# Kernel tuning notes

Hardware: AMD Instinct MI355X
Metric: run time of the kernel (lower is better)

Reference implementation:

```python
import jax, jax.numpy as jnp
import numpy as np

SIZES = [6890, 1723, 431, 108, 27]
P = [s + 1 for s in SIZES]  # padding vertex at each level
SPIRAL = 9
ENC_IN = [3, 16, 32, 64]; ENC_OUT = [16, 32, 64, 128]
DEC_IN = [128, 64, 32, 32, 16]; DEC_OUT = [64, 32, 32, 16, 3]
LATENT = 128
B = 64


def setup_inputs() -> dict:
    ks = iter(jax.random.split(jax.random.key(0), 80))
    def nrm(shape, scale=1.0):
        return jax.random.normal(next(ks), shape, dtype=jnp.float32) * scale
    inp = {'x': nrm((B, P[0], 3))}
    for l in range(4):
        inp['S%d' % l] = jax.random.randint(next(ks), (P[l], SPIRAL), 0, P[l], dtype=jnp.int32)
        inp['D%d' % l] = nrm((P[l + 1], P[l]), float(1.0 / np.sqrt(P[l])))
        inp['U%d' % l] = nrm((P[l], P[l + 1]), float(1.0 / np.sqrt(P[l + 1])))
    for i, (ci, co) in enumerate(zip(ENC_IN, ENC_OUT)):
        inp['W_e%d' % i] = nrm((ci * SPIRAL, co), float(1.0 / np.sqrt(ci * SPIRAL)))
        inp['b_e%d' % i] = nrm((co,), 0.02)
    inp['W_fe'] = nrm((P[4] * ENC_OUT[-1], LATENT), float(1.0 / np.sqrt(P[4] * ENC_OUT[-1])))
    inp['b_fe'] = nrm((LATENT,), 0.02)
    inp['W_fd'] = nrm((LATENT, P[4] * DEC_IN[0]), float(1.0 / np.sqrt(LATENT)))
    inp['b_fd'] = nrm((P[4] * DEC_IN[0],), 0.02)
    for i, (ci, co) in enumerate(zip(DEC_IN, DEC_OUT)):
        inp['W_d%d' % i] = nrm((ci * SPIRAL, co), float(1.0 / np.sqrt(ci * SPIRAL)))
        inp['b_d%d' % i] = nrm((co,), 0.02)
    return inp


def _sconv(x, idx, W, b, act):
    # spiral gather: x[B,P,F], idx[P,S] -> [B,P,S*F]; Linear + activation + zero last (padding) vertex
    Bn, Pn, F = x.shape
    g = x[:, idx, :].reshape(Bn, Pn, -1)
    y = act(g @ W + b)
    return y.at[:, -1, :].set(0.0)


def _forward(x, S, D, U, We, be, W_fe, b_fe, W_fd, b_fd, Wd, bd):
    elu = jax.nn.elu
    h = x
    for i in range(4):  # encoder: spiral conv then downsample
        h = _sconv(h, S[i], We[i], be[i], elu)
        h = jnp.einsum('pq,bqf->bpf', D[i], h)
    z = h.reshape(h.shape[0], -1) @ W_fe + b_fe
    h = (z @ W_fd + b_fd).reshape(z.shape[0], P[4], DEC_IN[0])
    for i in range(4):  # decoder: upsample then spiral conv
        h = jnp.einsum('pq,bqf->bpf', U[3 - i], h)
        h = _sconv(h, S[3 - i], Wd[i], bd[i], elu)
    h = _sconv(h, S[0], Wd[4], bd[4], lambda v: v)  # final identity-activation conv to xyz
    return h, z


def reference(x, S0, S1, S2, S3, D0, D1, D2, D3, U0, U1, U2, U3,
              W_e0, b_e0, W_e1, b_e1, W_e2, b_e2, W_e3, b_e3,
              W_fe, b_fe, W_fd, b_fd,
              W_d0, b_d0, W_d1, b_d1, W_d2, b_d2, W_d3, b_d3, W_d4, b_d4):
    return _forward(x, [S0, S1, S2, S3], [D0, D1, D2, D3], [U0, U1, U2, U3],
                    [W_e0, W_e1, W_e2, W_e3], [b_e0, b_e1, b_e2, b_e3],
                    W_fe, b_fe, W_fd, b_fd,
                    [W_d0, W_d1, W_d2, W_d3, W_d4], [b_d0, b_d1, b_d2, b_d3, b_d4])
```

## Files before the change

kernel.cpp:

```cpp
#include <hip/hip_runtime.h>
#include <math.h>

typedef unsigned short u16;
typedef _Float16 f16;
typedef __attribute__((ext_vector_type(8))) _Float16 f16x8;
typedef __attribute__((ext_vector_type(4))) float f32x4;
typedef float4 __attribute__((aligned(4))) float4u;

constexpr int P0 = 6891, P1 = 1724, P2 = 432, P3 = 109, P4 = 28;
constexpr int P0p = 6912;

constexpr size_t OFF_ZB   = 0;
constexpr size_t OFF_MD0  = OFF_ZB   + 256;
constexpr size_t OFF_MU0  = OFF_MD0  + (size_t)1792 * 6912 * 2;
constexpr size_t OFF_MD1  = OFF_MU0  + (size_t)6912 * 1792 * 2;
constexpr size_t OFF_MU1  = OFF_MD1  + (size_t)512 * 1792 * 2;
constexpr size_t OFF_MD2  = OFF_MU1  + (size_t)1792 * 512 * 2;
constexpr size_t OFF_MU2  = OFF_MD2  + (size_t)128 * 512 * 2;
constexpr size_t OFF_MD3  = OFF_MU2  + (size_t)512 * 128 * 2;
constexpr size_t OFF_MU3  = OFF_MD3  + (size_t)128 * 128 * 2;
constexpr size_t OFF_WE1  = OFF_MU3  + (size_t)128 * 128 * 2;
constexpr size_t OFF_WE2  = OFF_WE1  + (size_t)32 * 192 * 2;
constexpr size_t OFF_WE3  = OFF_WE2  + (size_t)64 * 320 * 2;
constexpr size_t OFF_WD0  = OFF_WE3  + (size_t)128 * 576 * 2;
constexpr size_t OFF_WD1  = OFF_WD0  + (size_t)64 * 1152 * 2;
constexpr size_t OFF_WD2  = OFF_WD1  + (size_t)32 * 576 * 2;
constexpr size_t OFF_WD3  = OFF_WD2  + (size_t)32 * 320 * 2;
constexpr size_t OFF_XT   = OFF_WD3  + (size_t)16 * 320 * 2;
constexpr size_t OFF_FCP  = OFF_XT   + (size_t)6912 * 64 * 3 * 4;
constexpr size_t OFF_B0   = OFF_FCP  + (size_t)28 * 8192 * 4;
constexpr size_t OFF_B1   = OFF_B0   + (size_t)1024 * 6912 * 2;
constexpr size_t OFF_PB   = OFF_B1   + (size_t)6912 * 2048 * 2;
constexpr size_t OFF_END  = OFF_PB   + (size_t)14680064;

constexpr int CN_MD0 = 1792 * 864, CN_MU0 = 6912 * 224, CN_MD1 = 512 * 224,
              CN_MU1 = 1792 * 64, CN_MD2 = 128 * 64, CN_MU2 = 512 * 16,
              CN_MD3 = 128 * 16, CN_MU3 = 128 * 16,
              CN_W1 = 32 * 24, CN_W2 = 64 * 40, CN_W3 = 128 * 72,
              CN_V0 = 64 * 144, CN_V1 = 32 * 72, CN_V2 = 32 * 40, CN_V3 = 16 * 40,
              CN_XT = 6912 * 64, CN_ZB = 32;
constexpr int CN_TOTAL = CN_MD0 + CN_MU0 + CN_MD1 + CN_MU1 + CN_MD2 + CN_MU2 +
                         CN_MD3 + CN_MU3 + CN_W1 + CN_W2 + CN_W3 + CN_V0 + CN_V1 +
                         CN_V2 + CN_V3 + CN_XT + CN_ZB;

__device__ __forceinline__ u16 f2h(float v) {
  f16 h = (f16)v;
  return __builtin_bit_cast(u16, h);
}
__device__ __forceinline__ float h2f(u16 u) {
  return (float)__builtin_bit_cast(f16, u);
}
__device__ __forceinline__ float eluf(float v) { return v > 0.f ? v : expm1f(v); }

__device__ __forceinline__ void gload16(const void* g, void* lds) {
  __builtin_amdgcn_global_load_lds(
      (const __attribute__((address_space(1))) unsigned int*)g,
      (__attribute__((address_space(3))) unsigned int*)lds, 16, 0, 0);
}

struct PrepSrc {
  const float *D0, *U0, *D1, *U1, *D2, *U2, *D3, *U3;
  const float *We1, *We2, *We3, *Wd0, *Wd1, *Wd2, *Wd3;
  const float *x;
};

__device__ __forceinline__ void conv_m_item(const float* __restrict__ M, u16* __restrict__ out,
                                            int idx, int P, int Q, int Qpad) {
  int cpr = Qpad >> 3;
  int p = idx / cpr, cq = idx - p * cpr;
  int w0 = (cq << 3) & ~63;
  int q0 = w0 + (((cq & 7) ^ (p & 7)) << 3);
  uint4 pk;
  if (p < P && q0 + 8 <= Q) {
    const float* s = M + (size_t)p * Q + q0;
    float4 va = *(const float4u*)s;
    float4 vb = *(const float4u*)(s + 4);
    pk.x = f2h(va.x) | ((unsigned)f2h(va.y) << 16);
    pk.y = f2h(va.z) | ((unsigned)f2h(va.w) << 16);
    pk.z = f2h(vb.x) | ((unsigned)f2h(vb.y) << 16);
    pk.w = f2h(vb.z) | ((unsigned)f2h(vb.w) << 16);
  } else {
    u16 v[8];
#pragma unroll
    for (int j = 0; j < 8; ++j) {
      int q = q0 + j;
      float f = (p < P && q < Q) ? M[(size_t)p * Q + q] : 0.f;
      v[j] = f2h(f);
    }
    pk.x = v[0] | ((unsigned)v[1] << 16); pk.y = v[2] | ((unsigned)v[3] << 16);
    pk.z = v[4] | ((unsigned)v[5] << 16); pk.w = v[6] | ((unsigned)v[7] << 16);
  }
  *(uint4*)(out + ((size_t)idx << 3)) = pk;
}

__device__ __forceinline__ void conv_w_item(const float* __restrict__ W, u16* __restrict__ out,
                                            int idx, int K, int F, int Kpad) {
  int cpr = Kpad >> 3;
  int co = idx / cpr, ck = idx - co * cpr;
  int w0 = (ck << 3) & ~63;
  int k0 = w0 + (((ck & 7) ^ (co & 7)) << 3);
  u16 v[8];
#pragma unroll
  for (int j = 0; j < 8; ++j) {
    int k = k0 + j;
    float f = (k < K) ? W[(size_t)k * F + co] : 0.f;
    v[j] = f2h(f);
  }
  uint4 pk;
  pk.x = v[0] | ((unsigned)v[1] << 16); pk.y = v[2] | ((unsigned)v[3] << 16);
  pk.z = v[4] | ((unsigned)v[5] << 16); pk.w = v[6] | ((unsigned)v[7] << 16);
  *(uint4*)(out + ((size_t)idx << 3)) = pk;
}

__global__ __launch_bounds__(256) void kprep(PrepSrc a, char* __restrict__ ws) {
  int i = blockIdx.x * 256 + threadIdx.x;
  if (i >= CN_TOTAL) return;
  if (i < CN_MD0) { conv_m_item(a.D0, (u16*)(ws + OFF_MD0), i, P1, P0, 6912); return; }
  i -= CN_MD0;
  if (i < CN_MU0) { conv_m_item(a.U0, (u16*)(ws + OFF_MU0), i, P0, P1, 1792); return; }
  i -= CN_MU0;
  if (i < CN_XT) {
    float* xt = (float*)(ws + OFF_XT);
    int p = i >> 6, b = i & 63;
    float v0 = 0, v1 = 0, v2 = 0;
    if (p < P0) { const float* s = a.x + ((size_t)b * P0 + p) * 3; v0 = s[0]; v1 = s[1]; v2 = s[2]; }
    float* d = xt + (size_t)i * 3;
    d[0] = v0; d[1] = v1; d[2] = v2;
    return;
  }
  i -= CN_XT;
  if (i < CN_MD1) { conv_m_item(a.D1, (u16*)(ws + OFF_MD1), i, P2, P1, 1792); return; }
  i -= CN_MD1;
  if (i < CN_MU1) { conv_m_item(a.U1, (u16*)(ws + OFF_MU1), i, P1, P2, 512); return; }
  i -= CN_MU1;
  if (i < CN_MD2) { conv_m_item(a.D2, (u16*)(ws + OFF_MD2), i, P3, P2, 512); return; }
  i -= CN_MD2;
  if (i < CN_MU2) { conv_m_item(a.U2, (u16*)(ws + OFF_MU2), i, P2, P3, 128); return; }
  i -= CN_MU2;
  if (i < CN_MD3) { conv_m_item(a.D3, (u16*)(ws + OFF_MD3), i, P4, P3, 128); return; }
  i -= CN_MD3;
  if (i < CN_MU3) { conv_m_item(a.U3, (u16*)(ws + OFF_MU3), i, P3, P4, 128); return; }
  i -= CN_MU3;
  if (i < CN_W1) { conv_w_item(a.We1, (u16*)(ws + OFF_WE1), i, 144, 32, 192); return; }
  i -= CN_W1;
  if (i < CN_W2) { conv_w_item(a.We2, (u16*)(ws + OFF_WE2), i, 288, 64, 320); return; }
  i -= CN_W2;
  if (i < CN_W3) { conv_w_item(a.We3, (u16*)(ws + OFF_WE3), i, 576, 128, 576); return; }
  i -= CN_W3;
  if (i < CN_V0) { conv_w_item(a.Wd0, (u16*)(ws + OFF_WD0), i, 1152, 64, 1152); return; }
  i -= CN_V0;
  if (i < CN_V1) { conv_w_item(a.Wd1, (u16*)(ws + OFF_WD1), i, 576, 32, 576); return; }
  i -= CN_V1;
  if (i < CN_V2) { conv_w_item(a.Wd2, (u16*)(ws + OFF_WD2), i, 288, 32, 320); return; }
  i -= CN_V2;
  if (i < CN_V3) { conv_w_item(a.Wd3, (u16*)(ws + OFF_WD3), i, 288, 16, 320); return; }
  i -= CN_V3;
  ((unsigned long long*)(ws + OFF_ZB))[i] = 0ull;
}

__global__ __launch_bounds__(256) void ksconv0(const float* __restrict__ xt, const int* __restrict__ S,
                                               const float* __restrict__ W, const float* __restrict__ bias,
                                               u16* __restrict__ out) {
  __shared__ float Wl[432];
  __shared__ float bl[16];
  int t = threadIdx.x;
  for (int i = t; i < 432; i += 256) Wl[i] = W[i];
  if (t < 16) bl[t] = bias[t];
  __syncthreads();
  int co = t >> 4, bI = blockIdx.y * 16 + (t & 15);
  int n = bI * 16 + co;
  size_t rowb = (size_t)n * P0p;
  int key = n & 7;
  int pstart = blockIdx.x * 64;
  for (int pc = 0; pc < 8; ++pc) {
    u16 h8[8];
#pragma unroll
    for (int j = 0; j < 8; ++j) {
      int p = pstart + pc * 8 + j;
      float a = bl[co];
      if (p < P0) {
        for (int s = 0; s < 9; ++s) {
          int idx = S[p * 9 + s];
          const float* xr = xt + ((size_t)idx * 64 + bI) * 3;
          a = fmaf(xr[0], Wl[(s * 3 + 0) * 16 + co], a);
          a = fmaf(xr[1], Wl[(s * 3 + 1) * 16 + co], a);
          a = fmaf(xr[2], Wl[(s * 3 + 2) * 16 + co], a);
        }
        a = eluf(a);
      }
      if (p >= P0 - 1) a = 0.f;
      h8[j] = f2h(a);
    }
    int p8 = pstart + pc * 8;
    int slot = ((p8 >> 3) & 7) ^ key;
    u16* dst = out + rowb + (p8 & ~63) + (slot << 3);
    uint4 pk;
    pk.x = h8[0] | ((unsigned)h8[1] << 16); pk.y = h8[2] | ((unsigned)h8[3] << 16);
    pk.z = h8[4] | ((unsigned)h8[5] << 16); pk.w = h8[6] | ((unsigned)h8[7] << 16);
    *(uint4*)dst = pk;
  }
}

template <bool GATHER, int TN, int LOG_FIN, bool DO_ELU>
__global__ __launch_bounds__(256) void kgemm(const u16* __restrict__ Asrc, const u16* __restrict__ Bsrc,
                                             const int* __restrict__ S, const float* __restrict__ bias,
                                             u16* __restrict__ Cout, const u16* __restrict__ zb,
                                             int Kpad, int Pn, int PpadC, int N) {
  constexpr int NF = TN / 16;
  __shared__ u16 Ash[2][128 * 64];
  __shared__ u16 Bsh[2][TN * 64];
  __shared__ int Sl[16 * 12];

  const int t = threadIdx.x, w = t >> 6, l = t & 63;
  int p0, b0 = 0, n0 = 0;
  if (GATHER) { p0 = blockIdx.x * 16; b0 = blockIdx.y * 8; n0 = blockIdx.z * TN; }
  else        { p0 = blockIdx.x * 128; n0 = blockIdx.y * 128; }

  if constexpr (GATHER) {
    for (int i = t; i < 144; i += 256) {
      int pp = p0 + i / 9;
      Sl[(i / 9) * 12 + (i % 9)] = (pp < Pn) ? S[pp * 9 + (i % 9)] : 0;
    }
    __syncthreads();
  }

  const int NK = Kpad >> 6;
  int NKs, ks0;
  if constexpr (GATHER) { NKs = NK; ks0 = 0; }
  else                  { NKs = NK / gridDim.z; ks0 = blockIdx.z * NKs; }
  f32x4 acc[2][NF];
#pragma unroll
  for (int a = 0; a < 2; ++a)
#pragma unroll
    for (int b = 0; b < NF; ++b) acc[a][b] = (f32x4){0.f, 0.f, 0.f, 0.f};

  auto stage = [&](int d, int ks) {
#pragma unroll
    for (int g0 = 0; g0 < 4; ++g0) {
      int g = g0 * 4 + w;
      int r = g * 8 + (l >> 3);
      const u16* src;
      if constexpr (GATHER) {
        int c = (l & 7) ^ (r & 7);
        int k = ks * 64 + c * 8;
        int s = k >> LOG_FIN;
        if (s < 9) {
          int kk = k & ((1 << LOG_FIN) - 1);
          int sv = Sl[(r & 15) * 12 + s];
          src = Asrc + (((sv << 6) + b0 + (r >> 4)) << LOG_FIN) + kk;
        } else src = zb;
      } else {
        src = Asrc + (size_t)(p0 + r) * Kpad + ks * 64 + (l & 7) * 8;
      }
      gload16(src, &Ash[d][g * 512]);
    }
#pragma unroll
    for (int g0 = 0; g0 < (TN / 8 + 3) / 4; ++g0) {
      int g = g0 * 4 + w;
      if (g < TN / 8) {
        int r = g * 8 + (l >> 3);
        const u16* src = Bsrc + (size_t)(n0 + r) * Kpad + ks * 64 + (l & 7) * 8;
        gload16(src, &Bsh[d][g * 512]);
      }
    }
  };

  auto compute = [&](int d) {
#pragma unroll
    for (int kh = 0; kh < 2; ++kh) {
      f16x8 av[2], bv[NF];
#pragma unroll
      for (int mf = 0; mf < 2; ++mf) {
        int r = w * 32 + mf * 16 + (l & 15);
        int c = kh * 4 + (l >> 4);
        av[mf] = *(const f16x8*)&Ash[d][r * 64 + ((c ^ (r & 7)) << 3)];
      }
#pragma unroll
      for (int nf = 0; nf < NF; ++nf) {
        int r = nf * 16 + (l & 15);
        int c = kh * 4 + (l >> 4);
        bv[nf] = *(const f16x8*)&Bsh[d][r * 64 + ((c ^ (r & 7)) << 3)];
      }
#pragma unroll
      for (int mf = 0; mf < 2; ++mf)
#pragma unroll
        for (int nf = 0; nf < NF; ++nf)
          acc[mf][nf] = __builtin_amdgcn_mfma_f32_16x16x32_f16(av[mf], bv[nf], acc[mf][nf], 0, 0, 0);
    }
  };

  stage(0, ks0);
  __syncthreads();
  for (int i = 0; i < NKs; ++i) {
    int d = i & 1;
    if (i + 1 < NKs) stage(d ^ 1, ks0 + i + 1);
    compute(d);
    __syncthreads();
  }

  if constexpr (GATHER) {
#pragma unroll
    for (int nf = 0; nf < NF; ++nf) {
      int co = n0 + nf * 16 + (l & 15);
      float bb = bias[co];
#pragma unroll
      for (int mf = 0; mf < 2; ++mf) {
        int b = b0 + w * 2 + mf;
        int n = b * N + co;
        int pbase = p0 + ((l >> 4) << 2);
        u16 hv[4];
#pragma unroll
        for (int rg = 0; rg < 4; ++rg) {
          float v = acc[mf][nf][rg] + bb;
          if (DO_ELU) v = eluf(v);
          if (pbase + rg >= Pn - 1) v = 0.f;
          hv[rg] = f2h(v);
        }
        int slot = ((pbase >> 3) & 7) ^ (n & 7);
        u16* dst = Cout + (size_t)n * PpadC + (pbase & ~63) + (slot << 3) + (pbase & 7);
        uint2 pk;
        pk.x = hv[0] | ((unsigned)hv[1] << 16);
        pk.y = hv[2] | ((unsigned)hv[3] << 16);
        *(uint2*)dst = pk;
      }
    }
  } else {
    u16* Cb = Cout + (size_t)blockIdx.z * ((size_t)gridDim.x * 128 * N);
#pragma unroll
    for (int mf = 0; mf < 2; ++mf) {
      int pb = p0 + w * 32 + mf * 16 + ((l >> 4) << 2);
#pragma unroll
      for (int nf = 0; nf < NF; ++nf) {
        int n = n0 + nf * 16 + (l & 15);
#pragma unroll
        for (int rg = 0; rg < 4; ++rg)
          Cb[(size_t)(pb + rg) * N + n] = f2h(acc[mf][nf][rg]);
      }
    }
  }
}

__global__ __launch_bounds__(256) void kred(const u16* __restrict__ part, u16* __restrict__ out,
                                            int mn8, int sk, size_t slice) {
  int i = blockIdx.x * 256 + threadIdx.x;
  if (i >= mn8) return;
  size_t base = (size_t)i * 8;
  float s[8] = {};
  for (int z = 0; z < sk; ++z) {
    uint4 u = *(const uint4*)(part + z * slice + base);
    s[0] += h2f((u16)u.x); s[1] += h2f((u16)(u.x >> 16));
    s[2] += h2f((u16)u.y); s[3] += h2f((u16)(u.y >> 16));
    s[4] += h2f((u16)u.z); s[5] += h2f((u16)(u.z >> 16));
    s[6] += h2f((u16)u.w); s[7] += h2f((u16)(u.w >> 16));
  }
  uint4 o;
  o.x = f2h(s[0]) | ((unsigned)f2h(s[1]) << 16);
  o.y = f2h(s[2]) | ((unsigned)f2h(s[3]) << 16);
  o.z = f2h(s[4]) | ((unsigned)f2h(s[5]) << 16);
  o.w = f2h(s[6]) | ((unsigned)f2h(s[7]) << 16);
  *(uint4*)(out + base) = o;
}

__global__ __launch_bounds__(256) void kfc_enc1(const u16* __restrict__ h, const float* __restrict__ W,
                                                float* __restrict__ partial) {
  __shared__ float hs[64][128];
  __shared__ float wsh[128][64];
  int p = blockIdx.x, nh = blockIdx.y, t = threadIdx.x;
  for (int i = t; i < 8192; i += 256) hs[i >> 7][i & 127] = h2f(h[(size_t)p * 8192 + i]);
  for (int i = t; i < 128 * 64; i += 256) {
    int kk = i >> 6, jj = i & 63;
    wsh[kk][jj] = W[(size_t)(p * 128 + kk) * 128 + nh * 64 + jj];
  }
  __syncthreads();
  int j = t & 63, bg = t >> 6;
  float acc[16] = {};
  for (int k = 0; k < 128; ++k) {
    float wv = wsh[k][j];
#pragma unroll
    for (int i = 0; i < 16; ++i) acc[i] = fmaf(hs[bg * 16 + i][k], wv, acc[i]);
  }
#pragma unroll
  for (int i = 0; i < 16; ++i)
    partial[((size_t)p * 64 + bg * 16 + i) * 128 + nh * 64 + j] = acc[i];
}

__global__ __launch_bounds__(256) void kfc_enc2(const float* __restrict__ partial,
                                                const float* __restrict__ bias, float* __restrict__ z) {
  int i = blockIdx.x * 256 + threadIdx.x;
  float a = bias[i & 127];
  for (int p = 0; p < 28; ++p) a += partial[(size_t)p * 8192 + i];
  z[i] = a;
}

__global__ __launch_bounds__(256) void kfc_dec(const float* __restrict__ z, const float* __restrict__ W,
                                               const float* __restrict__ bias, u16* __restrict__ out) {
  __shared__ float zs[8][128];
  int t = threadIdx.x, b0 = blockIdx.y * 8;
  for (int i = t; i < 8 * 128; i += 256) zs[i >> 7][i & 127] = z[(b0 + (i >> 7)) * 128 + (i & 127)];
  __syncthreads();
  int m = blockIdx.x * 256 + t;
  float bb = bias[m];
  float acc[8];
#pragma unroll
  for (int i = 0; i < 8; ++i) acc[i] = bb;
  for (int k = 0; k < 128; ++k) {
    float wv = W[(size_t)k * 3584 + m];
#pragma unroll
    for (int i = 0; i < 8; ++i) acc[i] = fmaf(zs[i][k], wv, acc[i]);
  }
  int p = m >> 7, f = m & 127;
  int slot0 = p >> 3;
#pragma unroll
  for (int i = 0; i < 8; ++i) {
    int n = (b0 + i) * 128 + f;
    int slot = slot0 ^ (n & 7);
    out[(size_t)n * 128 + (slot << 3) + (p & 7)] = f2h(acc[i]);
  }
}

__global__ __launch_bounds__(256) void ktr(const u16* __restrict__ fm, u16* __restrict__ vm,
                                           int Ppad, int Nn) {
  __shared__ u16 T[64][72];
  int p0 = blockIdx.x * 64, n0 = blockIdx.y * 64;
  int t = threadIdx.x;
  for (int it = 0; it < 2; ++it) {
    int id = t + it * 256;
    int r = id >> 3, slot = id & 7;
    int n = n0 + r;
    int c = slot ^ (n & 7);
    uint4 u = *(const uint4*)(fm + (size_t)n * Ppad + p0 + (slot << 3));
    T[c * 8 + 0][r] = (u16)u.x;  T[c * 8 + 1][r] = (u16)(u.x >> 16);
    T[c * 8 + 2][r] = (u16)u.y;  T[c * 8 + 3][r] = (u16)(u.y >> 16);
    T[c * 8 + 4][r] = (u16)u.z;  T[c * 8 + 5][r] = (u16)(u.z >> 16);
    T[c * 8 + 6][r] = (u16)u.w;  T[c * 8 + 7][r] = (u16)(u.w >> 16);
  }
  __syncthreads();
  for (int it = 0; it < 2; ++it) {
    int id = t + it * 256;
    int pr = id >> 3, ch = id & 7;
    uint4 pk;
    pk.x = T[pr][ch * 8 + 0] | ((unsigned)T[pr][ch * 8 + 1] << 16);
    pk.y = T[pr][ch * 8 + 2] | ((unsigned)T[pr][ch * 8 + 3] << 16);
    pk.z = T[pr][ch * 8 + 4] | ((unsigned)T[pr][ch * 8 + 5] << 16);
    pk.w = T[pr][ch * 8 + 6] | ((unsigned)T[pr][ch * 8 + 7] << 16);
    *(uint4*)(vm + (size_t)(p0 + pr) * Nn + n0 + (ch << 3)) = pk;
  }
}

__global__ __launch_bounds__(256) void kfinal(const u16* __restrict__ x, const int* __restrict__ S,
                                              const float* __restrict__ W, const float* __restrict__ bias,
                                              float* __restrict__ out) {
  __shared__ float Wl[432];
  __shared__ int Sl[64 * 9];
  int t = threadIdx.x;
  for (int i = t; i < 432; i += 256) Wl[i] = W[i];
  int pblk = blockIdx.x * 64;
  for (int i = t; i < 64 * 9; i += 256) {
    int pp = pblk + i / 9;
    Sl[i] = (pp < P0) ? S[pp * 9 + (i % 9)] : 0;
  }
  __syncthreads();
  int lane = t & 63, w = t >> 6;
  int p = pblk + lane;
  float b0v = bias[0], b1v = bias[1], b2v = bias[2];
  int idxs[9];
#pragma unroll
  for (int s = 0; s < 9; ++s) idxs[s] = Sl[lane * 9 + s];
#pragma unroll
  for (int bi = 0; bi < 2; ++bi) {
    int b = blockIdx.y * 8 + w * 2 + bi;
    float a0 = b0v, a1 = b1v, a2 = b2v;
    for (int s = 0; s < 9; ++s) {
      const f16x8* xr = (const f16x8*)(x + ((size_t)idxs[s] * 64 + b) * 16);
      f16x8 v0 = xr[0], v1 = xr[1];
#pragma unroll
      for (int j = 0; j < 8; ++j) {
        float xv = (float)v0[j];
        a0 = fmaf(xv, Wl[(s * 16 + j) * 3 + 0], a0);
        a1 = fmaf(xv, Wl[(s * 16 + j) * 3 + 1], a1);
        a2 = fmaf(xv, Wl[(s * 16 + j) * 3 + 2], a2);
      }
#pragma unroll
      for (int j = 0; j < 8; ++j) {
        float xv = (float)v1[j];
        a0 = fmaf(xv, Wl[(s * 16 + j + 8) * 3 + 0], a0);
        a1 = fmaf(xv, Wl[(s * 16 + j + 8) * 3 + 1], a1);
        a2 = fmaf(xv, Wl[(s * 16 + j + 8) * 3 + 2], a2);
      }
    }
    if (p < P0) {
      float* o = out + ((size_t)b * P0 + p) * 3;
      if (p == P0 - 1) { o[0] = 0.f; o[1] = 0.f; o[2] = 0.f; }
      else             { o[0] = a0;  o[1] = a1;  o[2] = a2; }
    }
  }
}

extern "C" void kernel_launch(void* const* d_in, const int* in_sizes, int n_in,
                              void* d_out, int out_size, void* d_ws, size_t ws_size,
                              hipStream_t stream) {
  (void)in_sizes; (void)n_in; (void)out_size;

  const float* x   = (const float*)d_in[0];
  const int*   S0  = (const int*)d_in[1];
  const float* D0  = (const float*)d_in[2];
  const float* U0  = (const float*)d_in[3];
  const int*   S1  = (const int*)d_in[4];
  const float* D1  = (const float*)d_in[5];
  const float* U1  = (const float*)d_in[6];
  const int*   S2  = (const int*)d_in[7];
  const float* D2  = (const float*)d_in[8];
  const float* U2  = (const float*)d_in[9];
  const int*   S3  = (const int*)d_in[10];
  const float* D3  = (const float*)d_in[11];
  const float* U3  = (const float*)d_in[12];
  const float* We0 = (const float*)d_in[13]; const float* be0 = (const float*)d_in[14];
  const float* We1 = (const float*)d_in[15]; const float* be1 = (const float*)d_in[16];
  const float* We2 = (const float*)d_in[17]; const float* be2 = (const float*)d_in[18];
  const float* We3 = (const float*)d_in[19]; const float* be3 = (const float*)d_in[20];
  const float* Wfe = (const float*)d_in[21]; const float* bfe = (const float*)d_in[22];
  const float* Wfd = (const float*)d_in[23]; const float* bfd = (const float*)d_in[24];
  const float* Wd0 = (const float*)d_in[25]; const float* bd0 = (const float*)d_in[26];
  const float* Wd1 = (const float*)d_in[27]; const float* bd1 = (const float*)d_in[28];
  const float* Wd2 = (const float*)d_in[29]; const float* bd2 = (const float*)d_in[30];
  const float* Wd3 = (const float*)d_in[31]; const float* bd3 = (const float*)d_in[32];
  const float* Wd4 = (const float*)d_in[33]; const float* bd4 = (const float*)d_in[34];

  char* ws = (char*)d_ws;
  u16*   zb   = (u16*)(ws + OFF_ZB);
  u16*   MbD0 = (u16*)(ws + OFF_MD0); u16* MbU0 = (u16*)(ws + OFF_MU0);
  u16*   MbD1 = (u16*)(ws + OFF_MD1); u16* MbU1 = (u16*)(ws + OFF_MU1);
  u16*   MbD2 = (u16*)(ws + OFF_MD2); u16* MbU2 = (u16*)(ws + OFF_MU2);
  u16*   MbD3 = (u16*)(ws + OFF_MD3); u16* MbU3 = (u16*)(ws + OFF_MU3);
  u16*   Wte1 = (u16*)(ws + OFF_WE1); u16* Wte2 = (u16*)(ws + OFF_WE2);
  u16*   Wte3 = (u16*)(ws + OFF_WE3); u16* Wtd0 = (u16*)(ws + OFF_WD0);
  u16*   Wtd1 = (u16*)(ws + OFF_WD1); u16* Wtd2 = (u16*)(ws + OFF_WD2);
  u16*   Wtd3 = (u16*)(ws + OFF_WD3);
  float* xt   = (float*)(ws + OFF_XT);
  float* fcp  = (float*)(ws + OFF_FCP);
  u16*   B0   = (u16*)(ws + OFF_B0);
  u16*   B1   = (u16*)(ws + OFF_B1);
  u16*   Pbuf = (u16*)(ws + OFF_PB);
  const bool sk = OFF_END <= ws_size;

  float* out_h = (float*)d_out;
  float* out_z = out_h + (size_t)64 * P0 * 3;

  auto cdiv = [](int a, int b) { return (a + b - 1) / b; };
  dim3 blk(256);

  auto rs = [&](const u16* Mb, const u16* Bin, int Mtiles, int Ntiles, int Kpad, int N, int SK) {
    if (sk && SK > 1) {
      kgemm<false, 128, 0, false><<<dim3(Mtiles, Ntiles, SK), blk, 0, stream>>>(
          Mb, Bin, nullptr, nullptr, Pbuf, zb, Kpad, 0, 0, N);
      int mn = Mtiles * 128 * N;
      kred<<<cdiv(mn / 8, 256), blk, 0, stream>>>(Pbuf, B1, mn / 8, SK, (size_t)mn);
    } else {
      kgemm<false, 128, 0, false><<<dim3(Mtiles, Ntiles), blk, 0, stream>>>(
          Mb, Bin, nullptr, nullptr, B1, zb, Kpad, 0, 0, N);
    }
  };

  PrepSrc ps{D0, U0, D1, U1, D2, U2, D3, U3, We1, We2, We3, Wd0, Wd1, Wd2, Wd3, x};
  kprep<<<cdiv(CN_TOTAL, 256), blk, 0, stream>>>(ps, ws);

  ksconv0<<<dim3(108, 4), blk, 0, stream>>>(xt, S0, We0, be0, B0);
  rs(MbD0, B0, 14, 8, 6912, 1024, 4);
  kgemm<true, 32, 4, true><<<dim3(112, 8), blk, 0, stream>>>(B1, Wte1, S1, be1, B0, zb, 192, P1, 1792, 32);
  rs(MbD1, B0, 4, 16, 1792, 2048, 7);
  kgemm<true, 64, 5, true><<<dim3(32, 8), blk, 0, stream>>>(B1, Wte2, S2, be2, B0, zb, 320, P2, 512, 64);
  rs(MbD2, B0, 1, 32, 512, 4096, 4);
  kgemm<true, 64, 6, true><<<dim3(8, 8, 2), blk, 0, stream>>>(B1, Wte3, S3, be3, B0, zb, 576, P3, 128, 128);
  rs(MbD3, B0, 1, 64, 128, 8192, 2);

  kfc_enc1<<<dim3(28, 2), blk, 0, stream>>>(B1, Wfe, fcp);
  kfc_enc2<<<dim3(32), blk, 0, stream>>>(fcp, bfe, out_z);
  kfc_dec<<<dim3(14, 8), blk, 0, stream>>>(out_z, Wfd, bfd, B0);

  rs(MbU3, B0, 1, 64, 128, 8192, 2);
  kgemm<true, 32, 7, true><<<dim3(8, 8, 2), blk, 0, stream>>>(B1, Wtd0, S3, bd0, B0, zb, 1152, P3, 128, 64);
  rs(MbU2, B0, 4, 32, 128, 4096, 2);
  kgemm<true, 32, 6, true><<<dim3(32, 8), blk, 0, stream>>>(B1, Wtd1, S2, bd1, B0, zb, 576, P2, 512, 32);
  rs(MbU1, B0, 14, 16, 512, 2048, 2);
  kgemm<true, 32, 5, true><<<dim3(112, 8), blk, 0, stream>>>(B1, Wtd2, S1, bd2, B0, zb, 320, P1, 1792, 32);
  rs(MbU0, B0, 54, 16, 1792, 2048, 1);
  kgemm<true, 16, 5, true><<<dim3(432, 8), blk, 0, stream>>>(B1, Wtd3, S0, bd3, B0, zb, 320, P0, 6912, 16);

  ktr<<<dim3(108, 16), blk, 0, stream>>>(B0, B1, 6912, 1024);
  kfinal<<<dim3(108, 8), blk, 0, stream>>>(B1, S0, Wd4, bd4, out_h);
}
```

Baseline: 467.5 us.

## Route first spiral conv through MFMA gemm, fuse FC reduce and drop transpose

The first encoder spiral conv is now a gather MFMA gemm over fp16 input padded to 8 channels, with matching padded weights. This replaces the scalar fp32 ksconv0 kernel. The FC encoder reduction is folded into kfc_dec, which removes one launch. The last decoder conv gains an output mode that writes vertex-major output through LDS, so the separate transpose kernel goes away. Several split-K factors on small decoder/encoder reductions drop from 2 to 1; the trade-offs are that more kernels depend on the fp16 path and some partial-reduction parallelism is lost.

```diff
diff --git a/kernel.cpp b/kernel.cpp
--- a/kernel.cpp
+++ b/kernel.cpp
@@ -26,8 +26,9 @@
 constexpr size_t OFF_WD1  = OFF_WD0  + (size_t)64 * 1152 * 2;
 constexpr size_t OFF_WD2  = OFF_WD1  + (size_t)32 * 576 * 2;
 constexpr size_t OFF_WD3  = OFF_WD2  + (size_t)32 * 320 * 2;
-constexpr size_t OFF_XT   = OFF_WD3  + (size_t)16 * 320 * 2;
-constexpr size_t OFF_FCP  = OFF_XT   + (size_t)6912 * 64 * 3 * 4;
+constexpr size_t OFF_WT0  = OFF_WD3  + (size_t)16 * 320 * 2;
+constexpr size_t OFF_XT   = OFF_WT0  + (size_t)16 * 128 * 2;
+constexpr size_t OFF_FCP  = OFF_XT   + (size_t)6912 * 64 * 8 * 2;
 constexpr size_t OFF_B0   = OFF_FCP  + (size_t)28 * 8192 * 4;
 constexpr size_t OFF_B1   = OFF_B0   + (size_t)1024 * 6912 * 2;
 constexpr size_t OFF_PB   = OFF_B1   + (size_t)6912 * 2048 * 2;
@@ -38,10 +39,10 @@
               CN_MD3 = 128 * 16, CN_MU3 = 128 * 16,
               CN_W1 = 32 * 24, CN_W2 = 64 * 40, CN_W3 = 128 * 72,
               CN_V0 = 64 * 144, CN_V1 = 32 * 72, CN_V2 = 32 * 40, CN_V3 = 16 * 40,
-              CN_XT = 6912 * 64, CN_ZB = 32;
+              CN_W0 = 16 * 16, CN_XT = 6912 * 64, CN_ZB = 32;
 constexpr int CN_TOTAL = CN_MD0 + CN_MU0 + CN_MD1 + CN_MU1 + CN_MD2 + CN_MU2 +
                          CN_MD3 + CN_MU3 + CN_W1 + CN_W2 + CN_W3 + CN_V0 + CN_V1 +
-                         CN_V2 + CN_V3 + CN_XT + CN_ZB;
+                         CN_V2 + CN_V3 + CN_W0 + CN_XT + CN_ZB;
 
 __device__ __forceinline__ u16 f2h(float v) {
   f16 h = (f16)v;
@@ -61,7 +62,7 @@
 struct PrepSrc {
   const float *D0, *U0, *D1, *U1, *D2, *U2, *D3, *U3;
   const float *We1, *We2, *We3, *Wd0, *Wd1, *Wd2, *Wd3;
-  const float *x;
+  const float *We0, *x;
 };
 
 __device__ __forceinline__ void conv_m_item(const float* __restrict__ M, u16* __restrict__ out,
@@ -112,6 +113,25 @@
   *(uint4*)(out + ((size_t)idx << 3)) = pk;
 }
 
+__device__ __forceinline__ void conv_w0_item(const float* __restrict__ W, u16* __restrict__ out,
+                                             int idx) {
+  int co = idx >> 4, ck = idx & 15;
+  int w0 = (ck << 3) & ~63;
+  int k0 = w0 + (((ck & 7) ^ (co & 7)) << 3);
+  u16 v[8];
+#pragma unroll
+  for (int j = 0; j < 8; ++j) {
+    int k = k0 + j;
+    int s = k >> 3, c = k & 7;
+    float f = (s < 9 && c < 3) ? W[(size_t)(s * 3 + c) * 16 + co] : 0.f;
+    v[j] = f2h(f);
+  }
+  uint4 pk;
+  pk.x = v[0] | ((unsigned)v[1] << 16); pk.y = v[2] | ((unsigned)v[3] << 16);
+  pk.z = v[4] | ((unsigned)v[5] << 16); pk.w = v[6] | ((unsigned)v[7] << 16);
+  *(uint4*)(out + ((size_t)idx << 3)) = pk;
+}
+
 __global__ __launch_bounds__(256) void kprep(PrepSrc a, char* __restrict__ ws) {
   int i = blockIdx.x * 256 + threadIdx.x;
   if (i >= CN_TOTAL) return;
@@ -120,12 +140,15 @@
   if (i < CN_MU0) { conv_m_item(a.U0, (u16*)(ws + OFF_MU0), i, P0, P1, 1792); return; }
   i -= CN_MU0;
   if (i < CN_XT) {
-    float* xt = (float*)(ws + OFF_XT);
+    u16* xt = (u16*)(ws + OFF_XT);
     int p = i >> 6, b = i & 63;
     float v0 = 0, v1 = 0, v2 = 0;
     if (p < P0) { const float* s = a.x + ((size_t)b * P0 + p) * 3; v0 = s[0]; v1 = s[1]; v2 = s[2]; }
-    float* d = xt + (size_t)i * 3;
-    d[0] = v0; d[1] = v1; d[2] = v2;
+    uint4 pk;
+    pk.x = f2h(v0) | ((unsigned)f2h(v1) << 16);
+    pk.y = f2h(v2);
+    pk.z = 0; pk.w = 0;
+    *(uint4*)(xt + ((size_t)i << 3)) = pk;
     return;
   }
   i -= CN_XT;
@@ -155,53 +178,12 @@
   i -= CN_V2;
   if (i < CN_V3) { conv_w_item(a.Wd3, (u16*)(ws + OFF_WD3), i, 288, 16, 320); return; }
   i -= CN_V3;
+  if (i < CN_W0) { conv_w0_item(a.We0, (u16*)(ws + OFF_WT0), i); return; }
+  i -= CN_W0;
   ((unsigned long long*)(ws + OFF_ZB))[i] = 0ull;
 }
 
-__global__ __launch_bounds__(256) void ksconv0(const float* __restrict__ xt, const int* __restrict__ S,
-                                               const float* __restrict__ W, const float* __restrict__ bias,
-                                               u16* __restrict__ out) {
-  __shared__ float Wl[432];
-  __shared__ float bl[16];
-  int t = threadIdx.x;
-  for (int i = t; i < 432; i += 256) Wl[i] = W[i];
-  if (t < 16) bl[t] = bias[t];
-  __syncthreads();
-  int co = t >> 4, bI = blockIdx.y * 16 + (t & 15);
-  int n = bI * 16 + co;
-  size_t rowb = (size_t)n * P0p;
-  int key = n & 7;
-  int pstart = blockIdx.x * 64;
-  for (int pc = 0; pc < 8; ++pc) {
-    u16 h8[8];
-#pragma unroll
-    for (int j = 0; j < 8; ++j) {
-      int p = pstart + pc * 8 + j;
-      float a = bl[co];
-      if (p < P0) {
-        for (int s = 0; s < 9; ++s) {
-          int idx = S[p * 9 + s];
-          const float* xr = xt + ((size_t)idx * 64 + bI) * 3;
-          a = fmaf(xr[0], Wl[(s * 3 + 0) * 16 + co], a);
-          a = fmaf(xr[1], Wl[(s * 3 + 1) * 16 + co], a);
-          a = fmaf(xr[2], Wl[(s * 3 + 2) * 16 + co], a);
-        }
-        a = eluf(a);
-      }
-      if (p >= P0 - 1) a = 0.f;
-      h8[j] = f2h(a);
-    }
-    int p8 = pstart + pc * 8;
-    int slot = ((p8 >> 3) & 7) ^ key;
-    u16* dst = out + rowb + (p8 & ~63) + (slot << 3);
-    uint4 pk;
-    pk.x = h8[0] | ((unsigned)h8[1] << 16); pk.y = h8[2] | ((unsigned)h8[3] << 16);
-    pk.z = h8[4] | ((unsigned)h8[5] << 16); pk.w = h8[6] | ((unsigned)h8[7] << 16);
-    *(uint4*)dst = pk;
-  }
-}
-
-template <bool GATHER, int TN, int LOG_FIN, bool DO_ELU>
+template <bool GATHER, int TN, int LOG_FIN, bool DO_ELU, int OUT_MODE = 0>
 __global__ __launch_bounds__(256) void kgemm(const u16* __restrict__ Asrc, const u16* __restrict__ Bsrc,
                                              const int* __restrict__ S, const float* __restrict__ bias,
                                              u16* __restrict__ Cout, const u16* __restrict__ zb,
@@ -247,7 +229,7 @@
         if (s < 9) {
           int kk = k & ((1 << LOG_FIN) - 1);
           int sv = Sl[(r & 15) * 12 + s];
-          src = Asrc + (((sv << 6) + b0 + (r >> 4)) << LOG_FIN) + kk;
+          src = Asrc + (((size_t)(sv << 6) + b0 + (r >> 4)) << LOG_FIN) + kk;
         } else src = zb;
       } else {
         src = Asrc + (size_t)(p0 + r) * Kpad + ks * 64 + (l & 7) * 8;
@@ -298,7 +280,27 @@
     __syncthreads();
   }
 
-  if constexpr (GATHER) {
+  if constexpr (GATHER && OUT_MODE == 1) {
+    u16* T = &Ash[0][0];
+    int co = l & 15;
+    float bb = bias[co];
+    int prow = (l >> 4) << 2;
+#pragma unroll
+    for (int mf = 0; mf < 2; ++mf) {
+      int ncol = (w * 2 + mf) * 16 + co;
+#pragma unroll
+      for (int rg = 0; rg < 4; ++rg) {
+        float v = acc[mf][0][rg] + bb;
+        if (DO_ELU) v = eluf(v);
+        if (p0 + prow + rg >= Pn - 1) v = 0.f;
+        T[(prow + rg) * 136 + ncol] = f2h(v);
+      }
+    }
+    __syncthreads();
+    int r = t >> 4, c8 = (t & 15) << 3;
+    uint4 pk = *(const uint4*)&T[r * 136 + c8];
+    *(uint4*)(Cout + (size_t)(p0 + r) * (64 * TN) + (size_t)blockIdx.y * 128 + c8) = pk;
+  } else if constexpr (GATHER) {
 #pragma unroll
     for (int nf = 0; nf < NF; ++nf) {
       int co = n0 + nf * 16 + (l & 15);
@@ -384,19 +386,19 @@
     partial[((size_t)p * 64 + bg * 16 + i) * 128 + nh * 64 + j] = acc[i];
 }
 
-__global__ __launch_bounds__(256) void kfc_enc2(const float* __restrict__ partial,
-                                                const float* __restrict__ bias, float* __restrict__ z) {
-  int i = blockIdx.x * 256 + threadIdx.x;
-  float a = bias[i & 127];
-  for (int p = 0; p < 28; ++p) a += partial[(size_t)p * 8192 + i];
-  z[i] = a;
-}
-
-__global__ __launch_bounds__(256) void kfc_dec(const float* __restrict__ z, const float* __restrict__ W,
+__global__ __launch_bounds__(256) void kfc_dec(const float* __restrict__ partial,
+                                               const float* __restrict__ bfe, float* __restrict__ z,
+                                               const float* __restrict__ W,
                                                const float* __restrict__ bias, u16* __restrict__ out) {
   __shared__ float zs[8][128];
   int t = threadIdx.x, b0 = blockIdx.y * 8;
-  for (int i = t; i < 8 * 128; i += 256) zs[i >> 7][i & 127] = z[(b0 + (i >> 7)) * 128 + (i & 127)];
+  for (int i = t; i < 8 * 128; i += 256) {
+    int bb = i >> 7, j = i & 127;
+    float s = bfe[j];
+    for (int p = 0; p < 28; ++p) s += partial[(size_t)p * 8192 + (b0 + bb) * 128 + j];
+    zs[bb][j] = s;
+    if (blockIdx.x == 0) z[(b0 + bb) * 128 + j] = s;
+  }
   __syncthreads();
   int m = blockIdx.x * 256 + t;
   float bb = bias[m];
@@ -415,35 +417,6 @@
     int n = (b0 + i) * 128 + f;
     int slot = slot0 ^ (n & 7);
     out[(size_t)n * 128 + (slot << 3) + (p & 7)] = f2h(acc[i]);
-  }
-}
-
-__global__ __launch_bounds__(256) void ktr(const u16* __restrict__ fm, u16* __restrict__ vm,
-                                           int Ppad, int Nn) {
-  __shared__ u16 T[64][72];
-  int p0 = blockIdx.x * 64, n0 = blockIdx.y * 64;
-  int t = threadIdx.x;
-  for (int it = 0; it < 2; ++it) {
-    int id = t + it * 256;
-    int r = id >> 3, slot = id & 7;
-    int n = n0 + r;
-    int c = slot ^ (n & 7);
-    uint4 u = *(const uint4*)(fm + (size_t)n * Ppad + p0 + (slot << 3));
-    T[c * 8 + 0][r] = (u16)u.x;  T[c * 8 + 1][r] = (u16)(u.x >> 16);
-    T[c * 8 + 2][r] = (u16)u.y;  T[c * 8 + 3][r] = (u16)(u.y >> 16);
-    T[c * 8 + 4][r] = (u16)u.z;  T[c * 8 + 5][r] = (u16)(u.z >> 16);
-    T[c * 8 + 6][r] = (u16)u.w;  T[c * 8 + 7][r] = (u16)(u.w >> 16);
-  }
-  __syncthreads();
-  for (int it = 0; it < 2; ++it) {
-    int id = t + it * 256;
-    int pr = id >> 3, ch = id & 7;
-    uint4 pk;
-    pk.x = T[pr][ch * 8 + 0] | ((unsigned)T[pr][ch * 8 + 1] << 16);
-    pk.y = T[pr][ch * 8 + 2] | ((unsigned)T[pr][ch * 8 + 3] << 16);
-    pk.z = T[pr][ch * 8 + 4] | ((unsigned)T[pr][ch * 8 + 5] << 16);
-    pk.w = T[pr][ch * 8 + 6] | ((unsigned)T[pr][ch * 8 + 7] << 16);
-    *(uint4*)(vm + (size_t)(p0 + pr) * Nn + n0 + (ch << 3)) = pk;
   }
 }
 
@@ -535,8 +508,8 @@
   u16*   Wte1 = (u16*)(ws + OFF_WE1); u16* Wte2 = (u16*)(ws + OFF_WE2);
   u16*   Wte3 = (u16*)(ws + OFF_WE3); u16* Wtd0 = (u16*)(ws + OFF_WD0);
   u16*   Wtd1 = (u16*)(ws + OFF_WD1); u16* Wtd2 = (u16*)(ws + OFF_WD2);
-  u16*   Wtd3 = (u16*)(ws + OFF_WD3);
-  float* xt   = (float*)(ws + OFF_XT);
+  u16*   Wtd3 = (u16*)(ws + OFF_WD3); u16* Wt0  = (u16*)(ws + OFF_WT0);
+  u16*   xt16 = (u16*)(ws + OFF_XT);
   float* fcp  = (float*)(ws + OFF_FCP);
   u16*   B0   = (u16*)(ws + OFF_B0);
   u16*   B1   = (u16*)(ws + OFF_B1);
@@ -561,31 +534,29 @@
     }
   };
 
-  PrepSrc ps{D0, U0, D1, U1, D2, U2, D3, U3, We1, We2, We3, Wd0, Wd1, Wd2, Wd3, x};
+  PrepSrc ps{D0, U0, D1, U1, D2, U2, D3, U3, We1, We2, We3, Wd0, Wd1, Wd2, Wd3, We0, x};
   kprep<<<cdiv(CN_TOTAL, 256), blk, 0, stream>>>(ps, ws);
 
-  ksconv0<<<dim3(108, 4), blk, 0, stream>>>(xt, S0, We0, be0, B0);
+  kgemm<true, 16, 3, true><<<dim3(432, 8), blk, 0, stream>>>(xt16, Wt0, S0, be0, B0, zb, 128, P0, P0p, 16);
   rs(MbD0, B0, 14, 8, 6912, 1024, 4);
   kgemm<true, 32, 4, true><<<dim3(112, 8), blk, 0, stream>>>(B1, Wte1, S1, be1, B0, zb, 192, P1, 1792, 32);
   rs(MbD1, B0, 4, 16, 1792, 2048, 7);
   kgemm<true, 64, 5, true><<<dim3(32, 8), blk, 0, stream>>>(B1, Wte2, S2, be2, B0, zb, 320, P2, 512, 64);
   rs(MbD2, B0, 1, 32, 512, 4096, 4);
   kgemm<true, 64, 6, true><<<dim3(8, 8, 2), blk, 0, stream>>>(B1, Wte3, S3, be3, B0, zb, 576, P3, 128, 128);
-  rs(MbD3, B0, 1, 64, 128, 8192, 2);
+  rs(MbD3, B0, 1, 64, 128, 8192, 1);
 
   kfc_enc1<<<dim3(28, 2), blk, 0, stream>>>(B1, Wfe, fcp);
-  kfc_enc2<<<dim3(32), blk, 0, stream>>>(fcp, bfe, out_z);
-  kfc_dec<<<dim3(14, 8), blk, 0, stream>>>(out_z, Wfd, bfd, B0);
-
-  rs(MbU3, B0, 1, 64, 128, 8192, 2);
+  kfc_dec<<<dim3(14, 8), blk, 0, stream>>>(fcp, bfe, out_z, Wfd, bfd, B0);
+
+  rs(MbU3, B0, 1, 64, 128, 8192, 1);
   kgemm<true, 32, 7, true><<<dim3(8, 8, 2), blk, 0, stream>>>(B1, Wtd0, S3, bd0, B0, zb, 1152, P3, 128, 64);
-  rs(MbU2, B0, 4, 32, 128, 4096, 2);
+  rs(MbU2, B0, 4, 32, 128, 4096, 1);
   kgemm<true, 32, 6, true><<<dim3(32, 8), blk, 0, stream>>>(B1, Wtd1, S2, bd1, B0, zb, 576, P2, 512, 32);
   rs(MbU1, B0, 14, 16, 512, 2048, 2);
   kgemm<true, 32, 5, true><<<dim3(112, 8), blk, 0, stream>>>(B1, Wtd2, S1, bd2, B0, zb, 320, P1, 1792, 32);
   rs(MbU0, B0, 54, 16, 1792, 2048, 1);
-  kgemm<true, 16, 5, true><<<dim3(432, 8), blk, 0, stream>>>(B1, Wtd3, S0, bd3, B0, zb, 320, P0, 6912, 16);
-
-  ktr<<<dim3(108, 16), blk, 0, stream>>>(B0, B1, 6912, 1024);
-  kfinal<<<dim3(108, 8), blk, 0, stream>>>(B1, S0, Wd4, bd4, out_h);
-}
+  kgemm<true, 16, 5, true, 1><<<dim3(432, 8), blk, 0, stream>>>(B1, Wtd3, S0, bd3, B0, zb, 320, P0, 0, 16);
+
+  kfinal<<<dim3(108, 8), blk, 0, stream>>>(B0, S0, Wd4, bd4, out_h);
+}
```

Result: faster. 415.6 us (-11.1%).
